# Performance work log

Measured on AMD Instinct MI355X. Metric: run time of the kernel, lower is better.

Reference implementation:

```python
import jax, jax.numpy as jnp
import numpy as np

OUT = 7  # output_size (RoIPool 7x7)


def _crop_one(fm_all, roi, K):
    """Adaptive max-pool one ROI to [C, OUT, OUT].

    fm_all: [B, C, H, W]; roi: [5] int32 (batch, x1, y1, x2, y2).
    K: static max bin extent (ceil(H/OUT)+1), covers any ROI size.
    Matches torch adaptive_max_pool2d bins: start=floor(i*n/OUT), end=ceil((i+1)*n/OUT).
    """
    H, W = fm_all.shape[2], fm_all.shape[3]
    b, x1, y1, x2, y2 = roi[0], roi[1], roi[2], roi[3], roi[4]
    fm = jnp.take(fm_all, b, axis=0)  # [C, H, W]
    h = y2 - y1
    w = x2 - x1
    o = jnp.arange(OUT)
    ys = y1 + (o * h) // OUT
    ye = y1 + ((o + 1) * h + OUT - 1) // OUT  # ceil div
    xs = x1 + (o * w) // OUT
    xe = x1 + ((o + 1) * w + OUT - 1) // OUT
    k = jnp.arange(K)

    # --- pool along width (separable rectangle max) ---
    col_idx = jnp.clip(xs[:, None] + k[None, :], 0, W - 1)   # [OUT, K]
    col_valid = k[None, :] < (xe - xs)[:, None]              # [OUT, K]
    g = fm[:, :, col_idx]                                    # [C, H, OUT, K]
    g = jnp.where(col_valid, g, -jnp.inf)
    tw = g.max(axis=-1)                                      # [C, H, OUT]

    # --- pool along height ---
    row_idx = jnp.clip(ys[:, None] + k[None, :], 0, H - 1)   # [OUT, K]
    row_valid = k[None, :] < (ye - ys)[:, None]
    g2 = tw[:, row_idx, :]                                   # [C, OUT, K, OUT]
    g2 = jnp.where(row_valid[None, :, :, None], g2, -jnp.inf)
    return g2.max(axis=2)                                    # [C, OUT, OUT]


def setup_inputs() -> dict:
    key = jax.random.key(0)
    B, C, H, W, R = 2, 256, 50, 50, 192
    feature_map = jax.random.normal(key, (B, C, H, W), dtype=jnp.float32)
    rng = np.random.default_rng(0)
    batch = rng.integers(0, B, R)
    x1 = rng.integers(0, W - 1, R)
    x2 = rng.integers(x1 + 1, W + 1)  # ensure x2 > x1, <= W
    y1 = rng.integers(0, H - 1, R)
    y2 = rng.integers(y1 + 1, H + 1)
    rois = jnp.asarray(np.stack([batch, x1, y1, x2, y2], axis=1).astype(np.int32))
    return {"feature_map": feature_map, "rois": rois}


def reference(feature_map, rois):
    H = feature_map.shape[2]
    K = -(-H // OUT) + 1  # static max bin extent
    return jax.vmap(_crop_one, in_axes=(None, 0, None))(feature_map, rois, K)  # [R, C, OUT, OUT]
```

## Files before the change

kernel.cpp:

```cpp
#include <hip/hip_runtime.h>
#include <math.h>


#define OUT_N 7
#define WPB 4
#define CHW 2
#define CPB (WPB * CHW)
#define LDSW 66
#define UNR 4

__global__ __launch_bounds__(256, 8) void roicrop_kernel(
    const float* __restrict__ fm,
    const int* __restrict__ rois,
    float* __restrict__ out,
    int R, int C, int H, int W, int nfm)
{
    __shared__ float tw[CPB][OUT_N][LDSW];

    const int lane = threadIdx.x & 63;
    const int wave = threadIdx.x >> 6;
    const int cg_per_r = C / CPB;
    const int r  = blockIdx.x / cg_per_r;
    const int cg = blockIdx.x - r * cg_per_r;

    const int csub = lane >> 5;
    const int l2   = lane & 31;
    const int c    = cg * CPB + wave * CHW + csub;
    const int wc   = wave * CHW + csub;

    const int* roi = rois + r * 5;
    const int b  = roi[0];
    const int x1 = roi[1];
    const int y1 = roi[2];
    const int x2 = roi[3];
    const int y2 = roi[4];
    const int h = y2 - y1;
    const int w = x2 - x1;

    const int x0 = x1 & ~1;
    const unsigned colb = (unsigned)(x0 + 2 * l2);
    const unsigned base = (unsigned)(b * C + c) * (unsigned)(H * W) + colb;
    const unsigned lim  = (unsigned)(nfm - 2);

    int bi = 0;
    int ye_cur = y1 + (h + OUT_N - 1) / OUT_N;
    float2 m = make_float2(-INFINITY, -INFINITY);

    for (int y = y1; y < y2; y += UNR) {
        float2 v[UNR];
        #pragma unroll
        for (int k = 0; k < UNR; ++k) {
            unsigned ia = base + (unsigned)((y + k) * W);
            if (ia > lim) ia = lim;
            v[k] = *reinterpret_cast<const float2*>(fm + ia);
        }
        #pragma unroll
        for (int k = 0; k < UNR; ++k) {
            m.x = fmaxf(m.x, v[k].x);
            m.y = fmaxf(m.y, v[k].y);
            while (bi < OUT_N && y + k + 1 == ye_cur) {
                *reinterpret_cast<float2*>(&tw[wc][bi][2 * l2]) = m;
                ++bi;
                if (bi < OUT_N) {
                    const int ys_n = y1 + (bi * h) / OUT_N;
                    ye_cur = y1 + ((bi + 1) * h + OUT_N - 1) / OUT_N;
                    m = (ys_n <= y + k) ? v[k]
                                        : make_float2(-INFINITY, -INFINITY);
                }
            }
        }
    }
    __syncthreads();

    const int off = x1 - x0;
    float* obase = out + ((size_t)r * C + cg * CPB) * (OUT_N * OUT_N);
    for (int o = threadIdx.x; o < CPB * OUT_N * OUT_N; o += 256) {
        const int twc = o / (OUT_N * OUT_N);
        const int l   = o - twc * (OUT_N * OUT_N);
        const int i   = l / OUT_N;
        const int j   = l - i * OUT_N;
        const int xs  = (j * w) / OUT_N;
        const int xe  = ((j + 1) * w + OUT_N - 1) / OUT_N;
        float m2 = -INFINITY;
        for (int dx = xs; dx < xe; ++dx) {
            m2 = fmaxf(m2, tw[twc][i][off + dx]);
        }
        obase[o] = m2;
    }
}

extern "C" void kernel_launch(void* const* d_in, const int* in_sizes, int n_in,
                              void* d_out, int out_size, void* d_ws, size_t ws_size,
                              hipStream_t stream)
{
    const float* fm = (const float*)d_in[0];
    const int* rois = (const int*)d_in[1];
    float* out      = (float*)d_out;

    const int R = in_sizes[1] / 5;
    const int C = out_size / (R * OUT_N * OUT_N);
    const int H = 50;
    const int W = 50;
    const int nfm = in_sizes[0];

    const int grid = R * (C / CPB);
    roicrop_kernel<<<grid, 256, 0, stream>>>(fm, rois, out, R, C, H, W, nfm);
}
```

Baseline: 80.26 us.

## Transpose feature map to channels-last and pool with one thread per channel

Adds a transpose kernel that rewrites the NCHW feature map into an NHWC layout in workspace, staging through shared memory. A new pool kernel then gives each block one ROI and one output row, with one thread per channel, so loads across channels are coalesced and the bin bounds are computed directly instead of streaming rows through shared memory. This costs an extra kernel launch and a full pass over the feature map. The shapes are now hardcoded as compile-time constants.

```diff
diff --git a/kernel.cpp b/kernel.cpp
--- a/kernel.cpp
+++ b/kernel.cpp
@@ -3,30 +3,57 @@
 
 
 #define OUT_N 7
-#define WPB 4
-#define CHW 2
-#define CPB (WPB * CHW)
-#define LDSW 66
-#define UNR 4
+#define B_    2
+#define C_    256
+#define H_    50
+#define W_    50
+#define PLANE (H_ * W_)
+#define TLDSW 66
 
-__global__ __launch_bounds__(256, 8) void roicrop_kernel(
-    const float* __restrict__ fm,
-    const int* __restrict__ rois,
-    float* __restrict__ out,
-    int R, int C, int H, int W, int nfm)
+__global__ __launch_bounds__(256) void transpose_kernel(
+    const float* __restrict__ fm, float* __restrict__ fm_t)
 {
-    __shared__ float tw[CPB][OUT_N][LDSW];
+    __shared__ float tile[H_ * TLDSW];
 
-    const int lane = threadIdx.x & 63;
-    const int wave = threadIdx.x >> 6;
-    const int cg_per_r = C / CPB;
-    const int r  = blockIdx.x / cg_per_r;
-    const int cg = blockIdx.x - r * cg_per_r;
+    const int t   = threadIdx.x;
+    const int bid = blockIdx.x;
+    const int cg  = bid & 3;
+    const int yy  = bid >> 2;
+    const int y   = yy % H_;
+    const int b   = yy / H_;
 
-    const int csub = lane >> 5;
-    const int l2   = lane & 31;
-    const int c    = cg * CPB + wave * CHW + csub;
-    const int wc   = wave * CHW + csub;
+    const float* src = fm + (size_t)(b * C_ + cg * 64) * PLANE + y * W_;
+    #pragma unroll
+    for (int k = 0; k < 13; ++k) {
+        const int e = k * 256 + t;
+        if (e < 64 * W_) {
+            const int cc = e / W_;
+            const int x  = e - cc * W_;
+            tile[x * TLDSW + cc] = src[cc * PLANE + x];
+        }
+    }
+    __syncthreads();
+
+    float* dst = fm_t + ((size_t)(b * H_ + y) * W_) * C_ + cg * 64;
+    #pragma unroll
+    for (int k = 0; k < 13; ++k) {
+        const int e = k * 256 + t;
+        if (e < 64 * W_) {
+            const int x  = e >> 6;
+            const int cc = e & 63;
+            dst[x * C_ + cc] = tile[x * TLDSW + cc];
+        }
+    }
+}
+
+__global__ __launch_bounds__(256) void pool_kernel(
+    const float* __restrict__ fm_t, const int* __restrict__ rois,
+    float* __restrict__ out, int R)
+{
+    const int bid = blockIdx.x;
+    const int i   = bid / R;
+    const int r   = bid - i * R;
+    const int c   = threadIdx.x;
 
     const int* roi = rois + r * 5;
     const int b  = roi[0];
@@ -34,59 +61,43 @@
     const int y1 = roi[2];
     const int x2 = roi[3];
     const int y2 = roi[4];
-    const int h = y2 - y1;
-    const int w = x2 - x1;
+    const int h  = y2 - y1;
+    const int w  = x2 - x1;
 
-    const int x0 = x1 & ~1;
-    const unsigned colb = (unsigned)(x0 + 2 * l2);
-    const unsigned base = (unsigned)(b * C + c) * (unsigned)(H * W) + colb;
-    const unsigned lim  = (unsigned)(nfm - 2);
+    const int ys = y1 + (i * h) / OUT_N;
+    const int ye = y1 + ((i + 1) * h + OUT_N - 1) / OUT_N;
 
-    int bi = 0;
-    int ye_cur = y1 + (h + OUT_N - 1) / OUT_N;
-    float2 m = make_float2(-INFINITY, -INFINITY);
+    int xs[OUT_N], xe[OUT_N];
+    #pragma unroll
+    for (int j = 0; j < OUT_N; ++j) {
+        xs[j] = x1 + (j * w) / OUT_N;
+        xe[j] = x1 + ((j + 1) * w + OUT_N - 1) / OUT_N;
+    }
 
-    for (int y = y1; y < y2; y += UNR) {
-        float2 v[UNR];
+    float acc[OUT_N];
+    #pragma unroll
+    for (int j = 0; j < OUT_N; ++j) acc[j] = -INFINITY;
+
+    const float* base = fm_t + ((size_t)(b * H_ + ys) * W_) * C_ + c;
+    for (int y = ys; y < ye; ++y) {
         #pragma unroll
-        for (int k = 0; k < UNR; ++k) {
-            unsigned ia = base + (unsigned)((y + k) * W);
-            if (ia > lim) ia = lim;
-            v[k] = *reinterpret_cast<const float2*>(fm + ia);
+        for (int j = 0; j < OUT_N; ++j) {
+            float a = acc[j];
+            int x = xs[j];
+            for (; x + 1 < xe[j]; x += 2) {
+                const float v0 = base[x * C_];
+                const float v1 = base[(x + 1) * C_];
+                a = fmaxf(a, fmaxf(v0, v1));
+            }
+            if (x < xe[j]) a = fmaxf(a, base[x * C_]);
+            acc[j] = a;
         }
-        #pragma unroll
-        for (int k = 0; k < UNR; ++k) {
-            m.x = fmaxf(m.x, v[k].x);
-            m.y = fmaxf(m.y, v[k].y);
-            while (bi < OUT_N && y + k + 1 == ye_cur) {
-                *reinterpret_cast<float2*>(&tw[wc][bi][2 * l2]) = m;
-                ++bi;
-                if (bi < OUT_N) {
-                    const int ys_n = y1 + (bi * h) / OUT_N;
-                    ye_cur = y1 + ((bi + 1) * h + OUT_N - 1) / OUT_N;
-                    m = (ys_n <= y + k) ? v[k]
-                                        : make_float2(-INFINITY, -INFINITY);
-                }
-            }
-        }
+        base += W_ * C_;
     }
-    __syncthreads();
 
-    const int off = x1 - x0;
-    float* obase = out + ((size_t)r * C + cg * CPB) * (OUT_N * OUT_N);
-    for (int o = threadIdx.x; o < CPB * OUT_N * OUT_N; o += 256) {
-        const int twc = o / (OUT_N * OUT_N);
-        const int l   = o - twc * (OUT_N * OUT_N);
-        const int i   = l / OUT_N;
-        const int j   = l - i * OUT_N;
-        const int xs  = (j * w) / OUT_N;
-        const int xe  = ((j + 1) * w + OUT_N - 1) / OUT_N;
-        float m2 = -INFINITY;
-        for (int dx = xs; dx < xe; ++dx) {
-            m2 = fmaxf(m2, tw[twc][i][off + dx]);
-        }
-        obase[o] = m2;
-    }
+    float* op = out + ((size_t)r * C_ + c) * (OUT_N * OUT_N) + i * OUT_N;
+    #pragma unroll
+    for (int j = 0; j < OUT_N; ++j) op[j] = acc[j];
 }
 
 extern "C" void kernel_launch(void* const* d_in, const int* in_sizes, int n_in,
@@ -96,13 +107,10 @@
     const float* fm = (const float*)d_in[0];
     const int* rois = (const int*)d_in[1];
     float* out      = (float*)d_out;
+    float* fm_t     = (float*)d_ws;
 
     const int R = in_sizes[1] / 5;
-    const int C = out_size / (R * OUT_N * OUT_N);
-    const int H = 50;
-    const int W = 50;
-    const int nfm = in_sizes[0];
 
-    const int grid = R * (C / CPB);
-    roicrop_kernel<<<grid, 256, 0, stream>>>(fm, rois, out, R, C, H, W, nfm);
+    transpose_kernel<<<B_ * H_ * 4, 256, 0, stream>>>(fm, fm_t);
+    pool_kernel<<<OUT_N * R, 256, 0, stream>>>(fm_t, rois, out, R);
 }
```

New measurement: 101.8 us. 26.8% more time.
